# Optimization experiments

Measured on AMD Instinct MI355X. Metric: run time of the kernel, lower is better.

## Reference

```python
import jax, jax.numpy as jnp
import numpy as np

LATENT = 64
HEADS = 4
N_A, N_B = 1024, 1024


def setup_inputs() -> dict:
    key = jax.random.key(0)
    ks = jax.random.split(key, 10)
    L = LATENT
    return {
        "rho_real": jax.random.normal(ks[0], (N_A, N_B), dtype=jnp.float32),
        "rho_imag": jax.random.normal(ks[1], (N_A, N_B), dtype=jnp.float32),
        "l_A": jax.random.randint(ks[2], (N_A,), 0, 3),
        "l_B": jax.random.randint(ks[3], (N_B,), 0, 3),
        "Z_A": 6,
        "Z_B": 8,
        # block_encoder: Linear(2, 64) -> SiLU -> Linear(64, latent_dim)
        "W1": jax.random.normal(ks[4], (64, 2), dtype=jnp.float32) * 0.5,
        "b1": jnp.zeros((64,), dtype=jnp.float32),
        "W2": jax.random.normal(ks[5], (L, 64), dtype=jnp.float32) * 0.1,
        "b2": jnp.zeros((L,), dtype=jnp.float32),
        # learned pooling query (1, latent_dim)
        "query": jax.random.normal(ks[6], (1, L), dtype=jnp.float32),
        # nn.MultiheadAttention packed in-projection and out-projection
        "in_proj_w": jax.random.normal(ks[7], (3 * L, L), dtype=jnp.float32) * 0.1,
        "in_proj_b": jnp.zeros((3 * L,), dtype=jnp.float32),
        "out_proj_w": jax.random.normal(ks[8], (L, L), dtype=jnp.float32) * 0.1,
        "out_proj_b": jnp.zeros((L,), dtype=jnp.float32),
    }


def reference(rho_real, rho_imag, l_A, l_B, Z_A, Z_B,
              W1, b1, W2, b2, query, in_proj_w, in_proj_b,
              out_proj_w, out_proj_b):
    L = query.shape[-1]
    H = HEADS
    hd = L // H
    # Batched equivalent of the per-(i,j) loop: all n_A*n_B elements at once.
    x = jnp.stack([rho_real.reshape(-1), rho_imag.reshape(-1)], axis=-1)  # [N, 2]
    h = jax.nn.silu(x @ W1.T + b1) @ W2.T + b2                            # [N, L]
    # MultiheadAttention with single query (batch=1, tgt_len=1, src_len=N)
    Wq, Wk, Wv = in_proj_w[:L], in_proj_w[L:2 * L], in_proj_w[2 * L:]
    bq, bk, bv = in_proj_b[:L], in_proj_b[L:2 * L], in_proj_b[2 * L:]
    q = (query @ Wq.T + bq).reshape(H, hd)        # [H, hd]
    k = (h @ Wk.T + bk).reshape(-1, H, hd)        # [N, H, hd]
    v = (h @ Wv.T + bv).reshape(-1, H, hd)        # [N, H, hd]
    scale = 1.0 / jnp.sqrt(jnp.asarray(hd, dtype=x.dtype))
    scores = jnp.einsum('hd,nhd->hn', q, k) * scale   # [H, N]
    attn = jax.nn.softmax(scores, axis=-1)
    pooled = jnp.einsum('hn,nhd->hd', attn, v).reshape(L)  # [L]
    return pooled @ out_proj_w.T + out_proj_b             # [latent_dim]
```

## Files before the change

### kernel.cpp

```cpp
#include <hip/hip_runtime.h>


#define LOG2E 1.44269504088896340736f
#define NLN2  (-0.69314718055994530942f)

#if __has_builtin(__builtin_amdgcn_exp2f)
#define EXP2(x) __builtin_amdgcn_exp2f(x)
#else
#define EXP2(x) exp2f(x)
#endif
#if __has_builtin(__builtin_amdgcn_rcpf)
#define RCP(x) __builtin_amdgcn_rcpf(x)
#else
#define RCP(x) (1.0f / (x))
#endif

#define WS_C4   0
#define WS_G4   256
#define WS_D    512
#define WS_ACC  768
#define NSLOT      16
#define SLOTSTRIDE 264

#define NPTS       (1024 * 1024)
#define NGROUPS    (NPTS / 64)
#define K1_BLOCKS  1024
#define K1_THREADS 128
#define WAVES_TOTAL (K1_BLOCKS * (K1_THREADS / 64))
#define GROUPS_PER_WAVE (NGROUPS / WAVES_TOTAL)

__global__ void setup_kernel(const float* __restrict__ W1, const float* __restrict__ b1,
                             const float* __restrict__ W2, const float* __restrict__ b2,
                             const float* __restrict__ query,
                             const float* __restrict__ ipw, const float* __restrict__ ipb,
                             float* __restrict__ ws)
{
    __shared__ float qs[64];
    __shared__ float as[4 * 64];
    const int t = threadIdx.x;

    for (int i = t; i < NSLOT * SLOTSTRIDE; i += 256) ws[WS_ACC + i] = 0.0f;

    if (t < 64) {
        float acc = ipb[t];
        for (int k = 0; k < 64; ++k) acc += ipw[t * 64 + k] * query[k];
        qs[t] = acc;
    }
    __syncthreads();

    {
        const int h = t >> 6, k = t & 63;
        float acc = 0.0f;
        for (int m = 0; m < 16; ++m)
            acc += ipw[(64 + h * 16 + m) * 64 + k] * qs[h * 16 + m];
        as[h * 64 + k] = 0.25f * acc;
    }
    __syncthreads();

    if (t < 64) {
        const int j = t;
        for (int h = 0; h < 4; ++h) {
            float g = 0.0f;
            for (int d = 0; d < 64; ++d) g += as[h * 64 + d] * W2[d * 64 + j];
            ws[WS_G4 + j * 4 + h] = LOG2E * g;
        }
        ws[WS_C4 + j * 4 + 0] = -LOG2E * W1[2 * j];
        ws[WS_C4 + j * 4 + 1] = -LOG2E * W1[2 * j + 1];
        ws[WS_C4 + j * 4 + 2] = -LOG2E * b1[j];
        ws[WS_C4 + j * 4 + 3] = 0.0f;
    }
    if (t < 4) {
        float d = 0.0f;
        for (int c = 0; c < 64; ++c) d += as[t * 64 + c] * b2[c];
        float qb = 0.0f;
        for (int m = 0; m < 16; ++m) qb += qs[t * 16 + m] * ipb[64 + t * 16 + m];
        ws[WS_D + t] = LOG2E * (d + 0.25f * qb);
    }
}

__global__ __launch_bounds__(K1_THREADS) void main_kernel(
        const float* __restrict__ rr, const float* __restrict__ ri,
        float* __restrict__ ws)
{
    __shared__ float4 c4s[64];
    __shared__ float4 g4s[64];
    __shared__ float  us[2][64 * 65];
    __shared__ float4 p4s[2][64];

    const int t    = threadIdx.x;
    const int lane = t & 63;
    const int w    = t >> 6;

    if (t < 64) c4s[t]       = ((const float4*)(ws + WS_C4))[t];
    else        g4s[t - 64]  = ((const float4*)(ws + WS_G4))[t - 64];
    const float d0 = ws[WS_D + 0], d1 = ws[WS_D + 1];
    const float d2 = ws[WS_D + 2], d3 = ws[WS_D + 3];
    __syncthreads();

    const int gwave = blockIdx.x * 2 + w;
    float l0 = 0, l1 = 0, l2 = 0, l3 = 0;
    float t0 = 0, t1 = 0, t2 = 0, t3 = 0;
    float* uw = us[w];

    for (int it = 0; it < GROUPS_PER_WAVE; ++it) {
        const int g   = gwave + it * WAVES_TOTAL;
        const int idx = g * 64 + lane;
        const float r  = rr[idx];
        const float im = ri[idx];

        float s0 = d0, s1 = d1, s2 = d2, s3 = d3;
        #pragma unroll 16
        for (int j = 0; j < 64; ++j) {
            const float4 c  = c4s[j];
            const float4 gg = g4s[j];
            const float zn = fmaf(c.x, r, fmaf(c.y, im, c.z));
            const float e  = EXP2(zn);
            const float rc = RCP(1.0f + e);
            const float u  = zn * NLN2 * rc;
            s0 = fmaf(gg.x, u, s0);
            s1 = fmaf(gg.y, u, s1);
            s2 = fmaf(gg.z, u, s2);
            s3 = fmaf(gg.w, u, s3);
            uw[j * 65 + lane] = u;
        }
        const float p0 = EXP2(s0), p1 = EXP2(s1), p2 = EXP2(s2), p3 = EXP2(s3);
        l0 += p0; l1 += p1; l2 += p2; l3 += p3;
        p4s[w][lane] = make_float4(p0, p1, p2, p3);
        __syncthreads();

        #pragma unroll 16
        for (int p = 0; p < 64; ++p) {
            const float  uu = uw[lane * 65 + p];
            const float4 pv = p4s[w][p];
            t0 = fmaf(pv.x, uu, t0);
            t1 = fmaf(pv.y, uu, t1);
            t2 = fmaf(pv.z, uu, t2);
            t3 = fmaf(pv.w, uu, t3);
        }
        __syncthreads();
    }

    for (int m = 1; m < 64; m <<= 1) {
        l0 += __shfl_xor(l0, m);
        l1 += __shfl_xor(l1, m);
        l2 += __shfl_xor(l2, m);
        l3 += __shfl_xor(l3, m);
    }

    float* acc = ws + WS_ACC + (blockIdx.x & (NSLOT - 1)) * SLOTSTRIDE;
    if (lane == 0) {
        atomicAdd(acc + 0, l0);
        atomicAdd(acc + 1, l1);
        atomicAdd(acc + 2, l2);
        atomicAdd(acc + 3, l3);
    }
    atomicAdd(acc + 4 + 0 * 64 + lane, t0);
    atomicAdd(acc + 4 + 1 * 64 + lane, t1);
    atomicAdd(acc + 4 + 2 * 64 + lane, t2);
    atomicAdd(acc + 4 + 3 * 64 + lane, t3);
}

__global__ void finish_kernel(const float* __restrict__ W2, const float* __restrict__ b2,
                              const float* __restrict__ ipw, const float* __restrict__ ipb,
                              const float* __restrict__ opw, const float* __restrict__ opb,
                              const float* __restrict__ ws, float* __restrict__ out)
{
    __shared__ float red[260];
    __shared__ float sb[256];
    __shared__ float pl[64];
    const int t = threadIdx.x;

    {
        float a = 0.0f;
        for (int s = 0; s < NSLOT; ++s) a += ws[WS_ACC + s * SLOTSTRIDE + t];
        red[t] = a;
        if (t < 4) {
            float a2 = 0.0f;
            for (int s = 0; s < NSLOT; ++s) a2 += ws[WS_ACC + s * SLOTSTRIDE + 256 + t];
            red[256 + t] = a2;
        }
    }
    __syncthreads();

    {
        const int h = t >> 6, j = t & 63;
        const float inv = 1.0f / red[h];
        float a = 0.0f;
        for (int k = 0; k < 64; ++k) a += W2[j * 64 + k] * red[4 + h * 64 + k];
        sb[t] = fmaf(inv, a, b2[j]);
    }
    __syncthreads();

    if (t < 64) {
        const int h = t >> 4;
        float a = ipb[128 + t];
        for (int d = 0; d < 64; ++d) a += ipw[(128 + t) * 64 + d] * sb[h * 64 + d];
        pl[t] = a;
    }
    __syncthreads();

    if (t < 64) {
        float a = opb[t];
        for (int p = 0; p < 64; ++p) a += opw[t * 64 + p] * pl[p];
        out[t] = a;
    }
}

extern "C" void kernel_launch(void* const* d_in, const int* in_sizes, int n_in,
                              void* d_out, int out_size, void* d_ws, size_t ws_size,
                              hipStream_t stream)
{
    const float* rr  = (const float*)d_in[0];
    const float* ri  = (const float*)d_in[1];
    const float* W1  = (const float*)d_in[6];
    const float* b1  = (const float*)d_in[7];
    const float* W2  = (const float*)d_in[8];
    const float* b2  = (const float*)d_in[9];
    const float* qy  = (const float*)d_in[10];
    const float* ipw = (const float*)d_in[11];
    const float* ipb = (const float*)d_in[12];
    const float* opw = (const float*)d_in[13];
    const float* opb = (const float*)d_in[14];
    float* ws  = (float*)d_ws;
    float* out = (float*)d_out;

    setup_kernel<<<1, 256, 0, stream>>>(W1, b1, W2, b2, qy, ipw, ipb, ws);
    main_kernel<<<K1_BLOCKS, K1_THREADS, 0, stream>>>(rr, ri, ws);
    finish_kernel<<<1, 256, 0, stream>>>(W2, b2, ipw, ipb, opw, opb, ws, out);
}
```

Measured before the change: 149.6 us.

## Store activations as bf16 in LDS, read constants from global, double grid size

The per-point SiLU activations staged in shared memory are now packed as rounded bf16 halves and read back two at a time. This halves LDS footprint and read traffic, so more blocks can sit on each CU. Constants are read straight from global/scalar memory instead of being copied to shared memory, and block barriers are swapped for workgroup fences since each wave only touches its own buffers. The grid is doubled and the accumulator slots increased, and zeroing moves to a memset. The cost is reduced precision in the value accumulation.

```diff
diff --git a/kernel.cpp b/kernel.cpp
--- a/kernel.cpp
+++ b/kernel.cpp
@@ -19,15 +19,17 @@
 #define WS_G4   256
 #define WS_D    512
 #define WS_ACC  768
-#define NSLOT      16
-#define SLOTSTRIDE 264
+#define NSLOT      32
+#define SLOTSTRIDE 272
 
 #define NPTS       (1024 * 1024)
 #define NGROUPS    (NPTS / 64)
-#define K1_BLOCKS  1024
+#define K1_BLOCKS  2048
 #define K1_THREADS 128
 #define WAVES_TOTAL (K1_BLOCKS * (K1_THREADS / 64))
 #define GROUPS_PER_WAVE (NGROUPS / WAVES_TOTAL)
+
+#define WG_FENCE() __builtin_amdgcn_fence(__ATOMIC_ACQ_REL, "workgroup")
 
 __global__ void setup_kernel(const float* __restrict__ W1, const float* __restrict__ b1,
                              const float* __restrict__ W2, const float* __restrict__ b2,
@@ -38,8 +40,6 @@
     __shared__ float qs[64];
     __shared__ float as[4 * 64];
     const int t = threadIdx.x;
-
-    for (int i = t; i < NSLOT * SLOTSTRIDE; i += 256) ws[WS_ACC + i] = 0.0f;
 
     if (t < 64) {
         float acc = ipb[t];
@@ -80,27 +80,22 @@
 
 __global__ __launch_bounds__(K1_THREADS) void main_kernel(
         const float* __restrict__ rr, const float* __restrict__ ri,
-        float* __restrict__ ws)
-{
-    __shared__ float4 c4s[64];
-    __shared__ float4 g4s[64];
-    __shared__ float  us[2][64 * 65];
+        const float4* __restrict__ c4g, const float4* __restrict__ g4g,
+        const float* __restrict__ dvec, float* __restrict__ accb)
+{
+    __shared__ unsigned short us[2][64 * 66];
     __shared__ float4 p4s[2][64];
 
     const int t    = threadIdx.x;
     const int lane = t & 63;
     const int w    = t >> 6;
 
-    if (t < 64) c4s[t]       = ((const float4*)(ws + WS_C4))[t];
-    else        g4s[t - 64]  = ((const float4*)(ws + WS_G4))[t - 64];
-    const float d0 = ws[WS_D + 0], d1 = ws[WS_D + 1];
-    const float d2 = ws[WS_D + 2], d3 = ws[WS_D + 3];
-    __syncthreads();
+    const float d0 = dvec[0], d1 = dvec[1], d2 = dvec[2], d3 = dvec[3];
 
     const int gwave = blockIdx.x * 2 + w;
     float l0 = 0, l1 = 0, l2 = 0, l3 = 0;
     float t0 = 0, t1 = 0, t2 = 0, t3 = 0;
-    float* uw = us[w];
+    unsigned short* uw = us[w];
 
     for (int it = 0; it < GROUPS_PER_WAVE; ++it) {
         const int g   = gwave + it * WAVES_TOTAL;
@@ -111,8 +106,8 @@
         float s0 = d0, s1 = d1, s2 = d2, s3 = d3;
         #pragma unroll 16
         for (int j = 0; j < 64; ++j) {
-            const float4 c  = c4s[j];
-            const float4 gg = g4s[j];
+            const float4 c  = c4g[j];
+            const float4 gg = g4g[j];
             const float zn = fmaf(c.x, r, fmaf(c.y, im, c.z));
             const float e  = EXP2(zn);
             const float rc = RCP(1.0f + e);
@@ -121,23 +116,28 @@
             s1 = fmaf(gg.y, u, s1);
             s2 = fmaf(gg.z, u, s2);
             s3 = fmaf(gg.w, u, s3);
-            uw[j * 65 + lane] = u;
+            uw[j * 66 + lane] =
+                (unsigned short)((__float_as_uint(u) + 0x8000u) >> 16);
         }
         const float p0 = EXP2(s0), p1 = EXP2(s1), p2 = EXP2(s2), p3 = EXP2(s3);
         l0 += p0; l1 += p1; l2 += p2; l3 += p3;
         p4s[w][lane] = make_float4(p0, p1, p2, p3);
-        __syncthreads();
-
+        WG_FENCE();
+
+        const unsigned int* urow = (const unsigned int*)(uw + lane * 66);
         #pragma unroll 16
-        for (int p = 0; p < 64; ++p) {
-            const float  uu = uw[lane * 65 + p];
-            const float4 pv = p4s[w][p];
-            t0 = fmaf(pv.x, uu, t0);
-            t1 = fmaf(pv.y, uu, t1);
-            t2 = fmaf(pv.z, uu, t2);
-            t3 = fmaf(pv.w, uu, t3);
-        }
-        __syncthreads();
+        for (int p2 = 0; p2 < 32; ++p2) {
+            const unsigned int bits = urow[p2];
+            const float ulo = __uint_as_float(bits << 16);
+            const float uhi = __uint_as_float(bits & 0xFFFF0000u);
+            const float4 pa = p4s[w][2 * p2];
+            const float4 pb = p4s[w][2 * p2 + 1];
+            t0 = fmaf(pa.x, ulo, t0); t0 = fmaf(pb.x, uhi, t0);
+            t1 = fmaf(pa.y, ulo, t1); t1 = fmaf(pb.y, uhi, t1);
+            t2 = fmaf(pa.z, ulo, t2); t2 = fmaf(pb.z, uhi, t2);
+            t3 = fmaf(pa.w, ulo, t3); t3 = fmaf(pb.w, uhi, t3);
+        }
+        WG_FENCE();
     }
 
     for (int m = 1; m < 64; m <<= 1) {
@@ -147,7 +147,7 @@
         l3 += __shfl_xor(l3, m);
     }
 
-    float* acc = ws + WS_ACC + (blockIdx.x & (NSLOT - 1)) * SLOTSTRIDE;
+    float* acc = accb + (blockIdx.x & (NSLOT - 1)) * SLOTSTRIDE;
     if (lane == 0) {
         atomicAdd(acc + 0, l0);
         atomicAdd(acc + 1, l1);
@@ -224,7 +224,11 @@
     float* ws  = (float*)d_ws;
     float* out = (float*)d_out;
 
+    hipMemsetAsync(ws + WS_ACC, 0, (size_t)NSLOT * SLOTSTRIDE * sizeof(float), stream);
     setup_kernel<<<1, 256, 0, stream>>>(W1, b1, W2, b2, qy, ipw, ipb, ws);
-    main_kernel<<<K1_BLOCKS, K1_THREADS, 0, stream>>>(rr, ri, ws);
+    main_kernel<<<K1_BLOCKS, K1_THREADS, 0, stream>>>(
+        rr, ri,
+        (const float4*)(ws + WS_C4), (const float4*)(ws + WS_G4),
+        ws + WS_D, ws + WS_ACC);
     finish_kernel<<<1, 256, 0, stream>>>(W2, b2, ipw, ipb, opw, opb, ws, out);
 }
```

Measured after the change: 139.2 us. 1.08x faster.
